# Kernel optimization log

Hardware: AMD Instinct MI355X
Metric: run time of the kernel (lower is better)

## Reference

```python
import jax, jax.numpy as jnp
import numpy as np

B, IN, H = 8192, 1024, 1024


def setup_inputs() -> dict:
    key = jax.random.key(0)
    ks = jax.random.split(key, 16)
    s_in = 1.0 / np.sqrt(IN)
    s_h = 1.0 / np.sqrt(H)
    d = {}
    d['x'] = jax.random.normal(ks[0], (B, IN), jnp.float32)
    d['h'] = jax.random.normal(ks[1], (B, H), jnp.float32)
    d['c_prev'] = jax.random.normal(ks[2], (B, H), jnp.float32)
    d['W_fx'] = jax.random.normal(ks[3], (H, IN), jnp.float32) * s_in
    d['b_f'] = jax.random.normal(ks[4], (H,), jnp.float32) * s_in
    d['W_fh'] = jax.random.normal(ks[5], (H, H), jnp.float32) * s_h
    d['W_ix'] = jax.random.normal(ks[6], (H, IN), jnp.float32) * s_in
    d['b_i'] = jax.random.normal(ks[7], (H,), jnp.float32) * s_in
    d['W_ih'] = jax.random.normal(ks[8], (H, H), jnp.float32) * s_h
    d['W_gx'] = jax.random.normal(ks[9], (H, IN), jnp.float32) * s_in
    d['b_g'] = jax.random.normal(ks[10], (H,), jnp.float32) * s_in
    d['W_gh'] = jax.random.normal(ks[11], (H, H), jnp.float32) * s_h
    d['W_ox'] = jax.random.normal(ks[12], (H, IN), jnp.float32) * s_in
    d['b_o'] = jax.random.normal(ks[13], (H,), jnp.float32) * s_in
    d['W_oh'] = jax.random.normal(ks[14], (H, H), jnp.float32) * s_h
    return d


def reference(x, h, c_prev, W_fx, b_f, W_fh, W_ix, b_i, W_ih,
              W_gx, b_g, W_gh, W_ox, b_o, W_oh):
    # Concatenate the four x-projections and four h-projections into two
    # fused GEMMs (same math as the 8 separate nn.Linear calls).
    Wx = jnp.concatenate([W_ix, W_fx, W_gx, W_ox], axis=0)  # [4H, IN]
    Wh = jnp.concatenate([W_ih, W_fh, W_gh, W_oh], axis=0)  # [4H, H]
    bx = jnp.concatenate([b_i, b_f, b_g, b_o], axis=0)       # [4H]
    z = x @ Wx.T + h @ Wh.T + bx                              # [B, 4H]
    zi, zf, zg, zo = jnp.split(z, 4, axis=-1)
    i = jax.nn.sigmoid(zi)
    f = jax.nn.sigmoid(zf)
    g = jnp.tanh(zg)
    o = jax.nn.sigmoid(zo)
    c_next = f * c_prev + i * g
    h_next = o * jnp.tanh(c_next)
    return (h_next, c_next)
```

## Files before the change

### kernel.cpp

```cpp
#include <hip/hip_runtime.h>
#include <stdint.h>

typedef unsigned short ushort_t;
typedef __attribute__((ext_vector_type(8))) short short8;
typedef __attribute__((ext_vector_type(4))) float floatx4;

#define B_   8192
#define IN_  1024
#define H_   1024

#define XB_ELEMS   (B_ * IN_)
#define WB_ELEMS   (H_ * IN_)
#define WS_XB   0
#define WS_HB   XB_ELEMS
#define WS_WB   (2 * XB_ELEMS)

__device__ __forceinline__ ushort_t f2bf(float f) {
    union { float f; uint32_t i; } v; v.f = f;
    uint32_t r = (v.i + 0x7fffu + ((v.i >> 16) & 1u)) >> 16;
    return (ushort_t)r;
}
__device__ __forceinline__ float sigmoid_(float x) {
    return 1.0f / (1.0f + __expf(-x));
}
__device__ __forceinline__ float tanh_(float x) {
    float xc = fminf(fmaxf(x, -20.f), 20.f);
    float e = __expf(2.f * xc);
    return (e - 1.f) / (e + 1.f);
}

__device__ __forceinline__ void gll16(const ushort_t* gsrc, ushort_t* ldst) {
    __builtin_amdgcn_global_load_lds(
        (const __attribute__((address_space(1))) void*)gsrc,
        (__attribute__((address_space(3))) void*)ldst,
        16, 0, 0);
}

__global__ __launch_bounds__(256) void cvt_kernel(
    const float* __restrict__ X,   const float* __restrict__ Hin,
    const float* __restrict__ Wix, const float* __restrict__ Wfx,
    const float* __restrict__ Wgx, const float* __restrict__ Wox,
    const float* __restrict__ Wih, const float* __restrict__ Wfh,
    const float* __restrict__ Wgh, const float* __restrict__ Woh,
    ushort_t* __restrict__ ws)
{
    const int c = blockIdx.x * 256 + threadIdx.x;
    const float* src;
    ushort_t* dst;
    int off;
    if (c < 2097152) {
        const int t = c >> 20;
        src = t ? Hin : X;
        dst = ws + (t ? WS_HB : WS_XB);
        off = (c & 1048575) * 8;
    } else {
        const int cc = c - 2097152;
        const int s = cc >> 17;
        const float* w =
            s == 0 ? Wix : s == 1 ? Wfx : s == 2 ? Wgx : s == 3 ? Wox :
            s == 4 ? Wih : s == 5 ? Wfh : s == 6 ? Wgh : Woh;
        src = w;
        dst = ws + WS_WB + s * WB_ELEMS;
        off = (cc & 131071) * 8;
    }
    float4 f0 = *(const float4*)(src + off);
    float4 f1 = *(const float4*)(src + off + 4);
    short8 o;
    o[0] = (short)f2bf(f0.x); o[1] = (short)f2bf(f0.y);
    o[2] = (short)f2bf(f0.z); o[3] = (short)f2bf(f0.w);
    o[4] = (short)f2bf(f1.x); o[5] = (short)f2bf(f1.y);
    o[6] = (short)f2bf(f1.z); o[7] = (short)f2bf(f1.w);
    *(short8*)(dst + off) = o;
}

__global__ __launch_bounds__(256) void lstm_cell_kernel(
    const ushort_t* __restrict__ Xb,  const ushort_t* __restrict__ Hb,
    const ushort_t* __restrict__ Wb,
    const float* __restrict__ Cprev,
    const float* __restrict__ Bi, const float* __restrict__ Bf,
    const float* __restrict__ Bg, const float* __restrict__ Bo,
    float* __restrict__ Out)
{
    __shared__ __align__(16) ushort_t As[128 * 64];
    __shared__ __align__(16) ushort_t Bs[128 * 64];

    const int t   = threadIdx.x;
    const int bm0 = blockIdx.y * 128;
    const int j0  = blockIdx.x * 32;

    int rA[4], kcA[4];
    const ushort_t* wxp[4];
    const ushort_t* whp[4];
    ushort_t *ldsA[4], *ldsB[4];
    #pragma unroll
    for (int i = 0; i < 4; ++i) {
        const int idx = t + 256 * i;
        rA[i]  = idx >> 3;
        const int p = idx & 7;
        kcA[i] = (p ^ (rA[i] & 7)) * 8;
        ldsA[i] = &As[idx * 8];
        ldsB[i] = &Bs[idx * 8];
        const int v = rA[i];
        const int g = (v >> 4) & 3;
        const int jj = j0 + ((v >> 6) << 4) + (v & 15);
        wxp[i] = Wb + (size_t)g * WB_ELEMS + (size_t)jj * IN_ + kcA[i];
        whp[i] = Wb + (size_t)(4 + g) * WB_ELEMS + (size_t)jj * H_ + kcA[i];
    }

    const int lane = t & 63;
    const int w = t >> 6;
    const int lr = lane & 15, lk = lane >> 4;
    const int rowbase = (w >> 1) * 64;
    const int colhalf = w & 1;

    floatx4 acc[4][4] = {};

    for (int phase = 0; phase < 2; ++phase) {
        const ushort_t* abase = phase ? Hb : Xb;
        const ushort_t* a0 = abase + (size_t)(bm0 + rA[0]) * IN_ + kcA[0];
        const ushort_t* a1 = abase + (size_t)(bm0 + rA[1]) * IN_ + kcA[1];
        const ushort_t* a2 = abase + (size_t)(bm0 + rA[2]) * IN_ + kcA[2];
        const ushort_t* a3 = abase + (size_t)(bm0 + rA[3]) * IN_ + kcA[3];
        const ushort_t* b0 = phase ? whp[0] : wxp[0];
        const ushort_t* b1 = phase ? whp[1] : wxp[1];
        const ushort_t* b2 = phase ? whp[2] : wxp[2];
        const ushort_t* b3 = phase ? whp[3] : wxp[3];
        for (int k0 = 0; k0 < 1024; k0 += 64) {
            gll16(a0, ldsA[0]); gll16(a1, ldsA[1]);
            gll16(a2, ldsA[2]); gll16(a3, ldsA[3]);
            gll16(b0, ldsB[0]); gll16(b1, ldsB[1]);
            gll16(b2, ldsB[2]); gll16(b3, ldsB[3]);
            a0 += 64; a1 += 64; a2 += 64; a3 += 64;
            b0 += 64; b1 += 64; b2 += 64; b3 += 64;
            __syncthreads();

            #pragma unroll
            for (int ks = 0; ks < 2; ++ks) {
                short8 af[4], bfr[4];
                #pragma unroll
                for (int rt = 0; rt < 4; ++rt) {
                    const int r = rowbase + rt * 16 + lr;
                    const int p = (ks * 4 + lk) ^ (r & 7);
                    af[rt] = *(const short8*)(&As[r * 64 + p * 8]);
                }
                #pragma unroll
                for (int ct = 0; ct < 4; ++ct) {
                    const int v = colhalf * 64 + ct * 16 + lr;
                    const int p = (ks * 4 + lk) ^ (v & 7);
                    bfr[ct] = *(const short8*)(&Bs[v * 64 + p * 8]);
                }
                #pragma unroll
                for (int rt = 0; rt < 4; ++rt)
                    #pragma unroll
                    for (int ct = 0; ct < 4; ++ct)
                        acc[rt][ct] = __builtin_amdgcn_mfma_f32_16x16x32_bf16(
                            af[rt], bfr[ct], acc[rt][ct], 0, 0, 0);
            }
            __syncthreads();
        }
    }

    const int j = j0 + colhalf * 16 + lr;
    const float bi = Bi[j], bff = Bf[j], bg = Bg[j], bo = Bo[j];

    #pragma unroll
    for (int rt = 0; rt < 4; ++rt) {
        #pragma unroll
        for (int reg = 0; reg < 4; ++reg) {
            const int m = bm0 + rowbase + rt * 16 + lk * 4 + reg;
            const float zi = acc[rt][0][reg] + bi;
            const float zf = acc[rt][1][reg] + bff;
            const float zg = acc[rt][2][reg] + bg;
            const float zo = acc[rt][3][reg] + bo;
            const float ig = sigmoid_(zi);
            const float fg = sigmoid_(zf);
            const float gg = tanh_(zg);
            const float og = sigmoid_(zo);
            const float cp = Cprev[(size_t)m * H_ + j];
            const float cn = fg * cp + ig * gg;
            const float hn = og * tanh_(cn);
            Out[(size_t)m * H_ + j] = hn;
            Out[(size_t)B_ * H_ + (size_t)m * H_ + j] = cn;
        }
    }
}

extern "C" void kernel_launch(void* const* d_in, const int* in_sizes, int n_in,
                              void* d_out, int out_size, void* d_ws, size_t ws_size,
                              hipStream_t stream)
{
    (void)in_sizes; (void)n_in; (void)out_size; (void)ws_size;
    const float* X   = (const float*)d_in[0];
    const float* Hin = (const float*)d_in[1];
    const float* Cp  = (const float*)d_in[2];
    const float* Wfx = (const float*)d_in[3];
    const float* Bf  = (const float*)d_in[4];
    const float* Wfh = (const float*)d_in[5];
    const float* Wix = (const float*)d_in[6];
    const float* Bi  = (const float*)d_in[7];
    const float* Wih = (const float*)d_in[8];
    const float* Wgx = (const float*)d_in[9];
    const float* Bg  = (const float*)d_in[10];
    const float* Wgh = (const float*)d_in[11];
    const float* Wox = (const float*)d_in[12];
    const float* Bo  = (const float*)d_in[13];
    const float* Woh = (const float*)d_in[14];
    float* Out = (float*)d_out;
    ushort_t* ws  = (ushort_t*)d_ws;

    cvt_kernel<<<dim3(12288), dim3(256), 0, stream>>>(
        X, Hin, Wix, Wfx, Wgx, Wox, Wih, Wfh, Wgh, Woh, ws);

    dim3 grid(H_ / 32, B_ / 128);
    lstm_cell_kernel<<<grid, dim3(256), 0, stream>>>(
        ws + WS_XB, ws + WS_HB, ws + WS_WB,
        Cp, Bi, Bf, Bg, Bo, Out);
}
```

Baseline: 332.9 us.

## Enlarge GEMM tile to 256x256 with double-buffered LDS and interleaved staging

Restructures the fused LSTM GEMM kernel to use 512-thread blocks computing 256 batch rows by 64 hidden units (256 gate columns). K-tiles are double-buffered in 128KB of LDS, with global-to-LDS loads for upcoming half-tiles issued between MFMA groups. The loop is split into quarter-tile phases using explicit barriers, waitcnt and setprio. This aims to raise arithmetic intensity and hide load latency. In exchange the block needs more LDS and registers (acc[8][4]), which limits occupancy, and the hand-tuned waitcnt sequencing is fragile.

```diff
diff --git a/kernel.cpp b/kernel.cpp
--- a/kernel.cpp
+++ b/kernel.cpp
@@ -73,7 +73,62 @@
     *(short8*)(dst + off) = o;
 }
 
-__global__ __launch_bounds__(256) void lstm_cell_kernel(
+
+#define BAR()  __builtin_amdgcn_s_barrier()
+#define LGKM0() do{ asm volatile("s_waitcnt lgkmcnt(0)" ::: "memory"); \
+                    __builtin_amdgcn_sched_barrier(0); }while(0)
+#define VMC(N) asm volatile("s_waitcnt vmcnt(" #N ")" ::: "memory")
+
+#define STAGE_A(TS, KH, DS) do{ \
+    const ushort_t* _s = (((TS) < 16) ? Xb : Hb) + (((TS) & 15) * 64 + (KH) * 32); \
+    ushort_t* _d = lds + ((DS) * 32768 + (KH) * 8192); \
+    gll16(_s + aoff0,          _d + t * 8); \
+    gll16(_s + aoff0 + 131072, _d + 4096 + t * 8); \
+  }while(0)
+
+#define STAGE_B(TS, KH, DS) do{ \
+    const ushort_t* _s = Wb + ((((TS) < 16) ? 0 : 4 * WB_ELEMS) + (((TS) & 15) * 64 + (KH) * 32)); \
+    ushort_t* _d = lds + ((DS) * 32768 + 16384 + (KH) * 8192); \
+    gll16(_s + boff0,         _d + t * 8); \
+    gll16(_s + boff0 + 32768, _d + 4096 + t * 8); \
+  }while(0)
+
+#define RD_A(S, KH, RF) (*(const short8*)(lds + ((S) * 32768 + (KH) * 8192) + a_rd + (RF) * 512))
+#define RD_B(S, KH, CT) (*(const short8*)(lds + ((S) * 32768 + 16384 + (KH) * 8192) + b_rd + (CT) * 512))
+
+#define MFMA16(RFB) do{ \
+    __builtin_amdgcn_s_setprio(1); \
+    _Pragma("unroll") \
+    for (int _rf = 0; _rf < 4; ++_rf) \
+      _Pragma("unroll") \
+      for (int _ct = 0; _ct < 4; ++_ct) \
+        acc[(RFB) + _rf][_ct] = __builtin_amdgcn_mfma_f32_16x16x32_bf16( \
+            af[_rf], bf[_ct], acc[(RFB) + _rf][_ct], 0, 0, 0); \
+    __builtin_amdgcn_s_setprio(0); \
+  }while(0)
+
+#define KTILE(T, S, ST01, ST23, VMSTMT) do{ \
+     \
+    _Pragma("unroll") for (int _r = 0; _r < 4; ++_r) af[_r] = RD_A(S, 0, _r); \
+    _Pragma("unroll") for (int _c = 0; _c < 4; ++_c) bf[_c] = RD_B(S, 0, _c); \
+    if (ST01) STAGE_A((T) + 1, 1, (S) ^ 1); \
+    BAR(); LGKM0(); MFMA16(0); BAR(); \
+     \
+    _Pragma("unroll") for (int _r = 0; _r < 4; ++_r) af[_r] = RD_A(S, 0, 4 + _r); \
+    if (ST01) STAGE_B((T) + 1, 1, (S) ^ 1); \
+    BAR(); LGKM0(); MFMA16(4); BAR(); \
+     \
+    _Pragma("unroll") for (int _r = 0; _r < 4; ++_r) af[_r] = RD_A(S, 1, _r); \
+    _Pragma("unroll") for (int _c = 0; _c < 4; ++_c) bf[_c] = RD_B(S, 1, _c); \
+    if (ST23) STAGE_A((T) + 2, 0, S); \
+    BAR(); LGKM0(); MFMA16(0); BAR(); \
+     \
+    _Pragma("unroll") for (int _r = 0; _r < 4; ++_r) af[_r] = RD_A(S, 1, 4 + _r); \
+    if (ST23) STAGE_B((T) + 2, 0, S); \
+    BAR(); LGKM0(); MFMA16(4); VMSTMT; BAR(); \
+  }while(0)
+
+__global__ __launch_bounds__(512, 2) void lstm_cell_kernel(
     const ushort_t* __restrict__ Xb,  const ushort_t* __restrict__ Hb,
     const ushort_t* __restrict__ Wb,
     const float* __restrict__ Cprev,
@@ -81,97 +136,55 @@
     const float* __restrict__ Bg, const float* __restrict__ Bo,
     float* __restrict__ Out)
 {
-    __shared__ __align__(16) ushort_t As[128 * 64];
-    __shared__ __align__(16) ushort_t Bs[128 * 64];
+    __shared__ __align__(16) ushort_t lds[65536];
 
     const int t   = threadIdx.x;
-    const int bm0 = blockIdx.y * 128;
-    const int j0  = blockIdx.x * 32;
-
-    int rA[4], kcA[4];
-    const ushort_t* wxp[4];
-    const ushort_t* whp[4];
-    ushort_t *ldsA[4], *ldsB[4];
+    const int bm0 = blockIdx.y * 256;
+    const int j0  = blockIdx.x * 64;
+
+    const int r0 = t >> 2;
+    const int c0 = (t & 3) ^ ((t >> 3) & 3);
+    const int aoff0 = (bm0 + r0) * 1024 + c0 * 8;
+    const int g0  = (r0 >> 4) & 3;
+    const int jv0 = j0 + ((r0 >> 6) << 4) + (r0 & 15);
+    const int boff0 = g0 * WB_ELEMS + jv0 * 1024 + c0 * 8;
+
+    const int lane = t & 63;
+    const int wid  = t >> 6;
+    const int wr = wid >> 2, wc = wid & 3;
+    const int lr = lane & 15, lk = lane >> 4;
+    const int xk = lk ^ ((lr >> 1) & 3);
+    const int a_rd = (wr * 512 + lr * 4 + xk) * 8;
+    const int b_rd = (wc * 256 + lr * 4 + xk) * 8;
+
+    short8 af[4], bf[4];
+    floatx4 acc[8][4] = {};
+
+    STAGE_A(0, 0, 0); STAGE_B(0, 0, 0);
+    STAGE_A(0, 1, 0); STAGE_B(0, 1, 0);
+    STAGE_A(1, 0, 1); STAGE_B(1, 0, 1);
+    VMC(4);
+    BAR();
+
+    for (int T = 0; T < 30; T += 2) {
+        KTILE(T,     0, 1, 1, VMC(4));
+        KTILE(T + 1, 1, 1, 1, VMC(4));
+    }
+    KTILE(30, 0, 1, 0, VMC(0));
+    KTILE(31, 1, 0, 0, (void)0);
+
+    const int j = j0 + wc * 16 + lr;
+    const float bi = Bi[j], bff = Bf[j], bg = Bg[j], bo = Bo[j];
+
     #pragma unroll
-    for (int i = 0; i < 4; ++i) {
-        const int idx = t + 256 * i;
-        rA[i]  = idx >> 3;
-        const int p = idx & 7;
-        kcA[i] = (p ^ (rA[i] & 7)) * 8;
-        ldsA[i] = &As[idx * 8];
-        ldsB[i] = &Bs[idx * 8];
-        const int v = rA[i];
-        const int g = (v >> 4) & 3;
-        const int jj = j0 + ((v >> 6) << 4) + (v & 15);
-        wxp[i] = Wb + (size_t)g * WB_ELEMS + (size_t)jj * IN_ + kcA[i];
-        whp[i] = Wb + (size_t)(4 + g) * WB_ELEMS + (size_t)jj * H_ + kcA[i];
-    }
-
-    const int lane = t & 63;
-    const int w = t >> 6;
-    const int lr = lane & 15, lk = lane >> 4;
-    const int rowbase = (w >> 1) * 64;
-    const int colhalf = w & 1;
-
-    floatx4 acc[4][4] = {};
-
-    for (int phase = 0; phase < 2; ++phase) {
-        const ushort_t* abase = phase ? Hb : Xb;
-        const ushort_t* a0 = abase + (size_t)(bm0 + rA[0]) * IN_ + kcA[0];
-        const ushort_t* a1 = abase + (size_t)(bm0 + rA[1]) * IN_ + kcA[1];
-        const ushort_t* a2 = abase + (size_t)(bm0 + rA[2]) * IN_ + kcA[2];
-        const ushort_t* a3 = abase + (size_t)(bm0 + rA[3]) * IN_ + kcA[3];
-        const ushort_t* b0 = phase ? whp[0] : wxp[0];
-        const ushort_t* b1 = phase ? whp[1] : wxp[1];
-        const ushort_t* b2 = phase ? whp[2] : wxp[2];
-        const ushort_t* b3 = phase ? whp[3] : wxp[3];
-        for (int k0 = 0; k0 < 1024; k0 += 64) {
-            gll16(a0, ldsA[0]); gll16(a1, ldsA[1]);
-            gll16(a2, ldsA[2]); gll16(a3, ldsA[3]);
-            gll16(b0, ldsB[0]); gll16(b1, ldsB[1]);
-            gll16(b2, ldsB[2]); gll16(b3, ldsB[3]);
-            a0 += 64; a1 += 64; a2 += 64; a3 += 64;
-            b0 += 64; b1 += 64; b2 += 64; b3 += 64;
-            __syncthreads();
-
-            #pragma unroll
-            for (int ks = 0; ks < 2; ++ks) {
-                short8 af[4], bfr[4];
-                #pragma unroll
-                for (int rt = 0; rt < 4; ++rt) {
-                    const int r = rowbase + rt * 16 + lr;
-                    const int p = (ks * 4 + lk) ^ (r & 7);
-                    af[rt] = *(const short8*)(&As[r * 64 + p * 8]);
-                }
-                #pragma unroll
-                for (int ct = 0; ct < 4; ++ct) {
-                    const int v = colhalf * 64 + ct * 16 + lr;
-                    const int p = (ks * 4 + lk) ^ (v & 7);
-                    bfr[ct] = *(const short8*)(&Bs[v * 64 + p * 8]);
-                }
-                #pragma unroll
-                for (int rt = 0; rt < 4; ++rt)
-                    #pragma unroll
-                    for (int ct = 0; ct < 4; ++ct)
-                        acc[rt][ct] = __builtin_amdgcn_mfma_f32_16x16x32_bf16(
-                            af[rt], bfr[ct], acc[rt][ct], 0, 0, 0);
-            }
-            __syncthreads();
-        }
-    }
-
-    const int j = j0 + colhalf * 16 + lr;
-    const float bi = Bi[j], bff = Bf[j], bg = Bg[j], bo = Bo[j];
-
-    #pragma unroll
-    for (int rt = 0; rt < 4; ++rt) {
+    for (int rf = 0; rf < 8; ++rf) {
         #pragma unroll
         for (int reg = 0; reg < 4; ++reg) {
-            const int m = bm0 + rowbase + rt * 16 + lk * 4 + reg;
-            const float zi = acc[rt][0][reg] + bi;
-            const float zf = acc[rt][1][reg] + bff;
-            const float zg = acc[rt][2][reg] + bg;
-            const float zo = acc[rt][3][reg] + bo;
+            const int m = bm0 + wr * 128 + rf * 16 + lk * 4 + reg;
+            const float zi = acc[rf][0][reg] + bi;
+            const float zf = acc[rf][1][reg] + bff;
+            const float zg = acc[rf][2][reg] + bg;
+            const float zo = acc[rf][3][reg] + bo;
             const float ig = sigmoid_(zi);
             const float fg = sigmoid_(zf);
             const float gg = tanh_(zg);
@@ -211,8 +224,8 @@
     cvt_kernel<<<dim3(12288), dim3(256), 0, stream>>>(
         X, Hin, Wix, Wfx, Wgx, Wox, Wih, Wfh, Wgh, Woh, ws);
 
-    dim3 grid(H_ / 32, B_ / 128);
-    lstm_cell_kernel<<<grid, dim3(256), 0, stream>>>(
+    dim3 grid(H_ / 64, B_ / 256);
+    lstm_cell_kernel<<<grid, dim3(512), 0, stream>>>(
         ws + WS_XB, ws + WS_HB, ws + WS_WB,
         Cp, Bi, Bf, Bg, Bo, Out);
 }
```

New measurement: 314.1 us. -5.7%, faster.
